# Optimization experiments

Hardware: AMD Instinct MI355X
Metric: run time of the kernel (lower is better)

The kernel has to match this reference:

```python
import jax, jax.numpy as jnp
import numpy as np

EPS = 1e-6

def setup_inputs() -> dict:
    key = jax.random.key(0)
    k1, k2 = jax.random.split(key)
    b, seq, d = 4, 512, 64
    x = jax.random.normal(k1, (b, seq, d, d), dtype=jnp.float32)
    # diagonal decay rates in (0, 1): realistic SSM decay, positive like the clamped param
    A = jax.random.uniform(k2, (d,), dtype=jnp.float32)
    return {"x": x, "A": A}

def reference(x, A):
    b, seq, d, _ = x.shape
    log_A = jnp.log(jnp.clip(A, EPS))                      # (d,)
    # cumsum over seq of the (constant-in-time) log decay, as in the original
    cs_A = jnp.cumsum(jnp.broadcast_to(log_A, (seq, d)), axis=0)  # (seq, d)
    log_M = cs_A[:, None, :] - cs_A[None, :, :]            # (t, j, d)
    idx = jnp.arange(seq)
    mask = idx[:, None] >= idx[None, :]                    # causal: t >= j
    M = jnp.where(mask[:, :, None], jnp.exp(log_M), 0.0)   # (t, j, d)
    # A is batch-independent, so M is shared across batch (same math as the original)
    out = jnp.einsum('tjr,bjrc->btrc', M, x)               # (b, seq, d, d)
    return out
```

## Files before the change

kernel.cpp:

```cpp
#include <hip/hip_runtime.h>


#define B_     4
#define SEQ_   512
#define D_     64
#define PLANE_ (D_ * D_)
#define PQ_    (PLANE_ / 4)
#define CH_    8
#define NCH_   (SEQ_ / CH_)
#define SPLIT_ 2
#define THR1_  (PQ_ / SPLIT_)

__global__ __launch_bounds__(THR1_) void ssm_k1_reduce(
    const float* __restrict__ x, const float* __restrict__ A,
    float* __restrict__ E)
{
    const int blk = blockIdx.x;
    const int h   = blk & (SPLIT_ - 1);
    const int m   = (blk >> 1) & (NCH_ - 1);
    const int b   = blk >> 7;
    const int k   = h * THR1_ + threadIdx.x;
    const int r   = k >> 4;

    const float a = fmaxf(A[r], 1e-6f);

    const float4* xp = (const float4*)x + (size_t)(b * SEQ_ + m * CH_) * PQ_ + k;

    float s0 = 0.f, s1 = 0.f, s2 = 0.f, s3 = 0.f;
#pragma unroll
    for (int t = 0; t < CH_; ++t) {
        float4 v = xp[t * PQ_];
        s0 = fmaf(s0, a, v.x);
        s1 = fmaf(s1, a, v.y);
        s2 = fmaf(s2, a, v.z);
        s3 = fmaf(s3, a, v.w);
    }
    ((float4*)E)[(size_t)(b * NCH_ + m) * PQ_ + k] = make_float4(s0, s1, s2, s3);
}

__global__ __launch_bounds__(64) void ssm_k2_carry(
    const float* __restrict__ A,
    const float* __restrict__ E, float* __restrict__ C)
{
    const int g = blockIdx.x * 64 + threadIdx.x;
    const int b = g >> 10;
    const int k = g & (PQ_ - 1);
    const int r = k >> 4;

    const float a  = fmaxf(A[r], 1e-6f);
    const float a2 = a * a, a4 = a2 * a2, aL = a4 * a4;

    const float4* Eb = (const float4*)E + (size_t)(b * NCH_) * PQ_ + k;
    float4*       Cb = (float4*)C       + (size_t)(b * NCH_) * PQ_ + k;

    float c0 = 0.f, c1 = 0.f, c2 = 0.f, c3 = 0.f;
#pragma unroll
    for (int m = 0; m < NCH_; ++m) {
        Cb[(size_t)m * PQ_] = make_float4(c0, c1, c2, c3);
        float4 e = Eb[(size_t)m * PQ_];
        c0 = fmaf(c0, aL, e.x);
        c1 = fmaf(c1, aL, e.y);
        c2 = fmaf(c2, aL, e.z);
        c3 = fmaf(c3, aL, e.w);
    }
}

__global__ __launch_bounds__(THR1_) void ssm_k3_fixup(
    const float* __restrict__ x, const float* __restrict__ A,
    const float* __restrict__ C, float* __restrict__ out)
{
    const int blk = blockIdx.x;
    const int h   = blk & (SPLIT_ - 1);
    const int m   = (blk >> 1) & (NCH_ - 1);
    const int b   = blk >> 7;
    const int k   = h * THR1_ + threadIdx.x;
    const int r   = k >> 4;

    const float a = fmaxf(A[r], 1e-6f);

    const float4* xp = (const float4*)x + (size_t)(b * SEQ_ + m * CH_) * PQ_ + k;
    float4*       op = (float4*)out     + (size_t)(b * SEQ_ + m * CH_) * PQ_ + k;

    float4 c4 = ((const float4*)C)[(size_t)(b * NCH_ + m) * PQ_ + k];
    float s0 = c4.x, s1 = c4.y, s2 = c4.z, s3 = c4.w;

#pragma unroll
    for (int t = 0; t < CH_; ++t) {
        float4 v = xp[t * PQ_];
        s0 = fmaf(s0, a, v.x);
        s1 = fmaf(s1, a, v.y);
        s2 = fmaf(s2, a, v.z);
        s3 = fmaf(s3, a, v.w);
        op[t * PQ_] = make_float4(s0, s1, s2, s3);
    }
}

#define CHF_ 32
#define NWF_ (SEQ_ / CHF_)
__global__ __launch_bounds__(NWF_ * 64) void ssm_fallback(
    const float* __restrict__ x, const float* __restrict__ A,
    float* __restrict__ out)
{
    __shared__ float Elds[NWF_ * D_];
    const int blk = blockIdx.x, bi = blk >> 6, r = blk & 63;
    const int tid = threadIdx.x, w = tid >> 6, c = tid & 63;
    const float a = fmaxf(A[r], 1e-6f);
    const size_t base = ((size_t)(bi * SEQ_ + w * CHF_) * D_ + r) * D_ + c;
    const float* xp = x + base;
    float*       op = out + base;
    const int js = D_ * D_;
    float local[CHF_];
    float state = 0.0f;
#pragma unroll
    for (int t = 0; t < CHF_; ++t) {
        state = fmaf(state, a, xp[(size_t)t * js]);
        local[t] = state;
    }
    Elds[w * D_ + c] = state;
    __syncthreads();
    float aL = a * a; aL *= aL; aL *= aL; aL *= aL; aL *= aL;
    float carry = 0.0f;
    for (int wp = 0; wp < w; ++wp) carry = fmaf(carry, aL, Elds[wp * D_ + c]);
    float p = a;
#pragma unroll
    for (int t = 0; t < CHF_; ++t) {
        op[(size_t)t * js] = fmaf(carry, p, local[t]);
        p *= a;
    }
}

extern "C" void kernel_launch(void* const* d_in, const int* in_sizes, int n_in,
                              void* d_out, int out_size, void* d_ws, size_t ws_size,
                              hipStream_t stream) {
    const float* x   = (const float*)d_in[0];
    const float* A   = (const float*)d_in[1];
    float*       out = (float*)d_out;

    const size_t planeBytes = sizeof(float) * (size_t)B_ * NCH_ * PLANE_;

    if (d_ws != nullptr && ws_size >= 2 * planeBytes) {
        float* E = (float*)d_ws;
        float* C = (float*)d_ws + (size_t)B_ * NCH_ * PLANE_;

        hipLaunchKernelGGL(ssm_k1_reduce, dim3(B_ * NCH_ * SPLIT_), dim3(THR1_),
                           0, stream, x, A, E);
        hipLaunchKernelGGL(ssm_k2_carry, dim3(B_ * PQ_ / 64), dim3(64),
                           0, stream, A, E, C);
        hipLaunchKernelGGL(ssm_k3_fixup, dim3(B_ * NCH_ * SPLIT_), dim3(THR1_),
                           0, stream, x, A, C, out);
    } else {
        hipLaunchKernelGGL(ssm_fallback, dim3(B_ * D_), dim3(NWF_ * 64),
                           0, stream, x, A, out);
    }
}
```

Before: 92.65 us.

## Fuse chunked scan into single kernel with decoupled-lookback flags

Replaces the three-kernel reduce/carry/fixup scan with one kernel. Each block computes its chunk's local scan, keeps it in registers, publishes the chunk sum with a release flag, then spins until all earlier chunks are published and folds their sums into a carry. This avoids reading x twice and drops the separate carry pass and its C buffer. In exchange it adds spin-waiting that can deadlock if earlier blocks are not resident, an O(m) serial carry loop per block, and a memset launch to clear the flags.

After: 244.6 us. +164.0%, slower.

```diff
diff --git a/kernel.cpp b/kernel.cpp
--- a/kernel.cpp
+++ b/kernel.cpp
@@ -9,23 +9,29 @@
 #define CH_    8
 #define NCH_   (SEQ_ / CH_)
 #define SPLIT_ 2
-#define THR1_  (PQ_ / SPLIT_)
+#define THR_   (PQ_ / SPLIT_)
+#define GRID_  (B_ * NCH_ * SPLIT_)
+#define NFLAGS_ GRID_
 
-__global__ __launch_bounds__(THR1_) void ssm_k1_reduce(
+__global__ __launch_bounds__(THR_, 4) void ssm_dlb(
     const float* __restrict__ x, const float* __restrict__ A,
-    float* __restrict__ E)
+    float* __restrict__ out, float* __restrict__ E,
+    int* __restrict__ flags)
 {
     const int blk = blockIdx.x;
     const int h   = blk & (SPLIT_ - 1);
     const int m   = (blk >> 1) & (NCH_ - 1);
     const int b   = blk >> 7;
-    const int k   = h * THR1_ + threadIdx.x;
+    const int k   = h * THR_ + threadIdx.x;
     const int r   = k >> 4;
 
-    const float a = fmaxf(A[r], 1e-6f);
+    const float a  = fmaxf(A[r], 1e-6f);
+    const float a2 = a * a, a4 = a2 * a2, aL = a4 * a4;
 
     const float4* xp = (const float4*)x + (size_t)(b * SEQ_ + m * CH_) * PQ_ + k;
+    float4*       op = (float4*)out     + (size_t)(b * SEQ_ + m * CH_) * PQ_ + k;
 
+    float4 loc[CH_];
     float s0 = 0.f, s1 = 0.f, s2 = 0.f, s3 = 0.f;
 #pragma unroll
     for (int t = 0; t < CH_; ++t) {
@@ -34,64 +40,50 @@
         s1 = fmaf(s1, a, v.y);
         s2 = fmaf(s2, a, v.z);
         s3 = fmaf(s3, a, v.w);
+        loc[t] = make_float4(s0, s1, s2, s3);
     }
-    ((float4*)E)[(size_t)(b * NCH_ + m) * PQ_ + k] = make_float4(s0, s1, s2, s3);
-}
 
-__global__ __launch_bounds__(64) void ssm_k2_carry(
-    const float* __restrict__ A,
-    const float* __restrict__ E, float* __restrict__ C)
-{
-    const int g = blockIdx.x * 64 + threadIdx.x;
-    const int b = g >> 10;
-    const int k = g & (PQ_ - 1);
-    const int r = k >> 4;
-
-    const float a  = fmaxf(A[r], 1e-6f);
-    const float a2 = a * a, a4 = a2 * a2, aL = a4 * a4;
-
-    const float4* Eb = (const float4*)E + (size_t)(b * NCH_) * PQ_ + k;
-    float4*       Cb = (float4*)C       + (size_t)(b * NCH_) * PQ_ + k;
+    if (m < NCH_ - 1) {
+        ((float4*)E)[(size_t)(b * NCH_ + m) * PQ_ + k] = make_float4(s0, s1, s2, s3);
+        __syncthreads();
+        if (threadIdx.x == 0) {
+            __threadfence();
+            __hip_atomic_store(&flags[blk], 1, __ATOMIC_RELEASE,
+                               __HIP_MEMORY_SCOPE_AGENT);
+        }
+    }
 
     float c0 = 0.f, c1 = 0.f, c2 = 0.f, c3 = 0.f;
-#pragma unroll
-    for (int m = 0; m < NCH_; ++m) {
-        Cb[(size_t)m * PQ_] = make_float4(c0, c1, c2, c3);
-        float4 e = Eb[(size_t)m * PQ_];
-        c0 = fmaf(c0, aL, e.x);
-        c1 = fmaf(c1, aL, e.y);
-        c2 = fmaf(c2, aL, e.z);
-        c3 = fmaf(c3, aL, e.w);
+    if (m > 0) {
+        const int fbase = (b * NCH_) * SPLIT_ + h;
+        for (;;) {
+            int allset = 1;
+            for (int mp = 0; mp < m; ++mp) {
+                allset &= (__hip_atomic_load(&flags[fbase + mp * SPLIT_],
+                           __ATOMIC_RELAXED, __HIP_MEMORY_SCOPE_AGENT) != 0);
+            }
+            if (allset) break;
+            __builtin_amdgcn_s_sleep(4);
+        }
+        __threadfence();
+
+        const float4* Eb = (const float4*)E + (size_t)(b * NCH_) * PQ_ + k;
+        for (int mp = 0; mp < m; ++mp) {
+            float4 e = Eb[(size_t)mp * PQ_];
+            c0 = fmaf(c0, aL, e.x);
+            c1 = fmaf(c1, aL, e.y);
+            c2 = fmaf(c2, aL, e.z);
+            c3 = fmaf(c3, aL, e.w);
+        }
     }
-}
 
-__global__ __launch_bounds__(THR1_) void ssm_k3_fixup(
-    const float* __restrict__ x, const float* __restrict__ A,
-    const float* __restrict__ C, float* __restrict__ out)
-{
-    const int blk = blockIdx.x;
-    const int h   = blk & (SPLIT_ - 1);
-    const int m   = (blk >> 1) & (NCH_ - 1);
-    const int b   = blk >> 7;
-    const int k   = h * THR1_ + threadIdx.x;
-    const int r   = k >> 4;
-
-    const float a = fmaxf(A[r], 1e-6f);
-
-    const float4* xp = (const float4*)x + (size_t)(b * SEQ_ + m * CH_) * PQ_ + k;
-    float4*       op = (float4*)out     + (size_t)(b * SEQ_ + m * CH_) * PQ_ + k;
-
-    float4 c4 = ((const float4*)C)[(size_t)(b * NCH_ + m) * PQ_ + k];
-    float s0 = c4.x, s1 = c4.y, s2 = c4.z, s3 = c4.w;
-
+    float p = a;
 #pragma unroll
     for (int t = 0; t < CH_; ++t) {
-        float4 v = xp[t * PQ_];
-        s0 = fmaf(s0, a, v.x);
-        s1 = fmaf(s1, a, v.y);
-        s2 = fmaf(s2, a, v.z);
-        s3 = fmaf(s3, a, v.w);
-        op[t * PQ_] = make_float4(s0, s1, s2, s3);
+        float4 l = loc[t];
+        op[t * PQ_] = make_float4(fmaf(c0, p, l.x), fmaf(c1, p, l.y),
+                                  fmaf(c2, p, l.z), fmaf(c3, p, l.w));
+        p *= a;
     }
 }
 
@@ -136,18 +128,15 @@
     const float* A   = (const float*)d_in[1];
     float*       out = (float*)d_out;
 
-    const size_t planeBytes = sizeof(float) * (size_t)B_ * NCH_ * PLANE_;
+    const size_t eBytes = sizeof(float) * (size_t)B_ * NCH_ * PLANE_;
+    const size_t fBytes = sizeof(int) * (size_t)NFLAGS_;
 
-    if (d_ws != nullptr && ws_size >= 2 * planeBytes) {
-        float* E = (float*)d_ws;
-        float* C = (float*)d_ws + (size_t)B_ * NCH_ * PLANE_;
-
-        hipLaunchKernelGGL(ssm_k1_reduce, dim3(B_ * NCH_ * SPLIT_), dim3(THR1_),
-                           0, stream, x, A, E);
-        hipLaunchKernelGGL(ssm_k2_carry, dim3(B_ * PQ_ / 64), dim3(64),
-                           0, stream, A, E, C);
-        hipLaunchKernelGGL(ssm_k3_fixup, dim3(B_ * NCH_ * SPLIT_), dim3(THR1_),
-                           0, stream, x, A, C, out);
+    if (d_ws != nullptr && ws_size >= eBytes + fBytes) {
+        float* E     = (float*)d_ws;
+        int*   flags = (int*)((char*)d_ws + eBytes);
+        hipMemsetAsync(flags, 0, fBytes, stream);
+        hipLaunchKernelGGL(ssm_dlb, dim3(GRID_), dim3(THR_), 0, stream,
+                           x, A, out, E, flags);
     } else {
         hipLaunchKernelGGL(ssm_fallback, dim3(B_ * D_), dim3(NWF_ * 64),
                            0, stream, x, A, out);
```
